# Optimization experiments

Measured on AMD Instinct MI355X. Metric: run time of the kernel, lower is better.

The kernel has to match this reference:

```python
import jax, jax.numpy as jnp
import numpy as np


def setup_inputs() -> dict:
    key = jax.random.key(0)
    ks = jax.random.split(key, 9)
    N, C, H, W, K = 8, 512, 64, 64, 32
    C4 = C // 4
    s = lambda k, shape, scale=0.02: jax.random.normal(k, shape, dtype=jnp.float32) * scale
    return {
        "x": jax.random.normal(ks[0], (N, C, H, W), dtype=jnp.float32),
        "y": jax.random.normal(ks[1], (N, K, C), dtype=jnp.float32),
        "wq": s(ks[2], (C4, C)),
        "bq": s(ks[3], (C4,)),
        "wk": s(ks[4], (C4, C)),
        "bk": s(ks[5], (C4,)),
        "wv": s(ks[6], (C, C)),
        "bv": s(ks[7], (C,)),
        "scale": s(ks[8], (1,), 1.0),
    }


def reference(x, y, wq, bq, wk, bk, wv, bv, scale):
    N, C, H, W = x.shape
    # 1x1 conv query: (N,C,H,W) -> (N,C4,H,W) -> (N, HW, C4)
    q = jnp.einsum('nchw,oc->nhwo', x, wq) + bq  # (N,H,W,C4)
    q = q.reshape(N, H * W, -1)                   # (N, HW, C4)
    # key/value linears on centers y: (N,K,C)
    k = y @ wk.T + bk                             # (N, K, C4)
    v = y @ wv.T + bv                             # (N, K, C)
    energy = jnp.einsum('npc,nkc->npk', q, k)     # (N, HW, K)
    attn = jax.nn.softmax(energy, axis=-1)
    out = jnp.einsum('nkc,npk->ncp', v, attn)     # (N, C, HW)
    out = out.reshape(N, C, H, W)
    return scale[0] * out + x
```

## Files before the change

### kernel.cpp

```cpp
#include <hip/hip_runtime.h>


#define N_  8
#define C_  512
#define HW_ 4096
#define K_  32

typedef __attribute__((ext_vector_type(8))) short bf16x8;
typedef __attribute__((ext_vector_type(4))) float f32x4;
typedef __attribute__((ext_vector_type(4))) int i32x4;

__device__ __forceinline__ unsigned short f2b(float f) {
    union { float f; unsigned u; } v; v.f = f;
    unsigned r = v.u + 0x7FFFu + ((v.u >> 16) & 1u);
    return (unsigned short)(r >> 16);
}

__device__ __forceinline__ int wqk_idx(int kk, int c) {
    return ((((c >> 5) * 2 + (kk >> 4)) * 64 + ((c >> 3) & 3) * 16 + (kk & 15)) << 3) + (c & 7);
}

__global__ __launch_bounds__(256) void prep_kernel(
    const float* __restrict__ y, const float* __restrict__ wq, const float* __restrict__ bq,
    const float* __restrict__ wk, const float* __restrict__ bk,
    const float* __restrict__ wv, const float* __restrict__ bv,
    unsigned short* __restrict__ wqkf, float* __restrict__ bqk, float* __restrict__ vp)
{
    const int bid = blockIdx.x;
    const int t = threadIdx.x;

    if (bid < 128) {
        const int n  = bid >> 4;
        const int ct = (bid >> 1) & 7;
        const int jh = bid & 1;
        const int cl = t & 63;
        const int c  = ct * 64 + cl;
        const int kko = __builtin_amdgcn_readfirstlane(t >> 6);

        const float* yb  = y  + ((size_t)n * K_ + kko * 8) * C_ + jh * 256;
        const float* wvb = wv + (size_t)c * C_ + jh * 256;
        float acc[8] = {0,0,0,0,0,0,0,0};
        for (int jq = 0; jq < 64; ++jq) {
            float4 w4 = *(const float4*)(wvb + jq * 4);
            #pragma unroll
            for (int u = 0; u < 8; ++u) {
                float4 y4 = *(const float4*)(yb + (size_t)u * C_ + jq * 4);
                acc[u] += y4.x * w4.x + y4.y * w4.y + y4.z * w4.z + y4.w * w4.w;
            }
        }
        const float bvc = (jh == 0) ? bv[c] : 0.0f;
        float* vpo = vp + (size_t)jh * N_ * K_ * C_;
        #pragma unroll
        for (int u = 0; u < 8; ++u)
            vpo[((size_t)n * K_ + kko * 8 + u) * C_ + c] = acc[u] + bvc;
    } else {
        __shared__ __align__(16) float kp[2][128];
        __shared__ __align__(16) float kr[128];
        const int b = bid - 128;
        const int n = b >> 5, kk = b & 31;
        const int o = t & 127, half = t >> 7;

        const float* yb  = y  + ((size_t)n * K_ + kk) * C_ + half * 256;
        const float* wkb = wk + (size_t)o * C_ + half * 256;
        float a = 0.f;
        for (int jq = 0; jq < 64; ++jq) {
            float4 w4 = *(const float4*)(wkb + jq * 4);
            float4 y4 = *(const float4*)(yb + jq * 4);
            a += y4.x * w4.x + y4.y * w4.y + y4.z * w4.z + y4.w * w4.w;
        }
        kp[half][o] = a;
        __syncthreads();
        if (t < 128) kr[t] = kp[0][t] + kp[1][t] + bk[t];
        __syncthreads();
        if (t < 64) {
            float s = kr[t] * bq[t] + kr[t + 64] * bq[t + 64];
            #pragma unroll
            for (int d = 32; d > 0; d >>= 1) s += __shfl_down(s, d);
            if (t == 0) bqk[n * K_ + kk] = s;
        }
        const int c1 = t, c2 = t + 256;
        float s1 = 0.f, s2 = 0.f;
        for (int oq = 0; oq < 32; ++oq) {
            float4 k4 = *(const float4*)(&kr[oq * 4]);
            const float* wq0 = wq + (size_t)(oq * 4) * C_;
            s1 += k4.x * wq0[c1] + k4.y * wq0[C_ + c1] + k4.z * wq0[2*C_ + c1] + k4.w * wq0[3*C_ + c1];
            s2 += k4.x * wq0[c2] + k4.y * wq0[C_ + c2] + k4.z * wq0[2*C_ + c2] + k4.w * wq0[3*C_ + c2];
        }
        unsigned short* wqf_n = wqkf + (size_t)n * (K_ * C_);
        wqf_n[wqk_idx(kk, c1)] = f2b(s1);
        wqf_n[wqk_idx(kk, c2)] = f2b(s2);
    }
}

__global__ __launch_bounds__(256) void pack_v_kernel(
    const float* __restrict__ vp, unsigned short* __restrict__ vtf)
{
    const int gid = blockIdx.x * 256 + threadIdx.x;
    const int n = gid >> 11, rem = gid & 2047;
    const int l = rem & 63;
    const int mt = rem >> 6;
    const int c = mt * 16 + (l & 15), g = l >> 4;
    const float* p0 = vp + ((size_t)n * K_ + g * 8) * C_ + c;
    const float* p1 = p0 + (size_t)N_ * K_ * C_;
    unsigned short o[8];
    #pragma unroll
    for (int j = 0; j < 8; ++j) o[j] = f2b(p0[(size_t)j * C_] + p1[(size_t)j * C_]);
    i32x4 pk = { (int)(o[0] | ((unsigned)o[1] << 16)), (int)(o[2] | ((unsigned)o[3] << 16)),
                 (int)(o[4] | ((unsigned)o[5] << 16)), (int)(o[6] | ((unsigned)o[7] << 16)) };
    *(i32x4*)(vtf + (size_t)n * (K_ * C_) + (size_t)rem * 8) = pk;
}

__global__ __launch_bounds__(512) void main_kernel(
    const float* __restrict__ x, const unsigned short* __restrict__ wqkf,
    const unsigned short* __restrict__ vtf, const float* __restrict__ bqk,
    const float* __restrict__ scale, float* __restrict__ out)
{
    __shared__ float e_lds[64][33];
    __shared__ __align__(16) unsigned short attnf[2048];

    const int bid = blockIdx.x;
    const int n  = bid >> 6;
    const int p0 = (bid & 63) * 64;
    const int t  = threadIdx.x;
    const int w  = t >> 6, l = t & 63;
    const int l15 = l & 15, lg = l >> 4;

    {
        const int pt = w & 3, kt = w >> 2;
        const unsigned short* wqf = wqkf + (size_t)n * (K_ * C_);
        const float* xc = x + (size_t)n * C_ * HW_ + p0 + pt * 16 + l15;

        float xr[8];
        #pragma unroll
        for (int u = 0; u < 8; ++u) xr[u] = xc[(size_t)(8 * lg + u) * HW_];
        bf16x8 bcur = *(const bf16x8*)(wqf + ((size_t)kt * 64 + l) * 8);

        f32x4 acc = {0.f, 0.f, 0.f, 0.f};
        for (int cs = 0; cs < 16; ++cs) {
            float xn[8];
            bf16x8 bnext;
            if (cs < 15) {
                #pragma unroll
                for (int u = 0; u < 8; ++u)
                    xn[u] = xc[(size_t)((cs + 1) * 32 + 8 * lg + u) * HW_];
                bnext = *(const bf16x8*)(wqf + ((size_t)((cs + 1) * 2 + kt) * 64 + l) * 8);
            }
            bf16x8 af;
            #pragma unroll
            for (int u = 0; u < 8; ++u) af[u] = (short)f2b(xr[u]);
            acc = __builtin_amdgcn_mfma_f32_16x16x32_bf16(af, bcur, acc, 0, 0, 0);
            #pragma unroll
            for (int u = 0; u < 8; ++u) xr[u] = xn[u];
            bcur = bnext;
        }
        const float bq_ = bqk[n * K_ + kt * 16 + l15];
        #pragma unroll
        for (int r = 0; r < 4; ++r)
            e_lds[pt * 16 + lg * 4 + r][kt * 16 + l15] = acc[r] + bq_;
    }
    __syncthreads();

    if (t < 64) {
        const int px = t;
        float e[32];
        #pragma unroll
        for (int k = 0; k < 32; ++k) e[k] = e_lds[px][k];
        float mx = e[0];
        #pragma unroll
        for (int k = 1; k < 32; ++k) mx = fmaxf(mx, e[k]);
        float s = 0.f;
        #pragma unroll
        for (int k = 0; k < 32; ++k) { e[k] = __expf(e[k] - mx); s += e[k]; }
        const float inv = 1.f / s;
        const int pt = px >> 4, c15 = px & 15;
        #pragma unroll
        for (int g = 0; g < 4; ++g) {
            i32x4 pk = { (int)(f2b(e[8*g+0]*inv) | ((unsigned)f2b(e[8*g+1]*inv) << 16)),
                         (int)(f2b(e[8*g+2]*inv) | ((unsigned)f2b(e[8*g+3]*inv) << 16)),
                         (int)(f2b(e[8*g+4]*inv) | ((unsigned)f2b(e[8*g+5]*inv) << 16)),
                         (int)(f2b(e[8*g+6]*inv) | ((unsigned)f2b(e[8*g+7]*inv) << 16)) };
            *(i32x4*)&attnf[(pt * 64 + g * 16 + c15) * 8] = pk;
        }
    }
    __syncthreads();

    {
        const int pt = w & 3, mh = w >> 2;
        const bf16x8 af = *(const bf16x8*)&attnf[(pt * 64 + l) * 8];
        const unsigned short* vtfn = vtf + (size_t)n * (K_ * C_);
        const float fs = scale[0];
        const int px = p0 + pt * 16 + l15;
        const float* xg = x + (size_t)n * C_ * HW_;
        float* og = out + (size_t)n * C_ * HW_;

        const int mt0 = mh * 16;
        bf16x8 vcur = *(const bf16x8*)(vtfn + ((size_t)mt0 * 64 + l) * 8);
        const int c0 = mt0 * 16 + lg * 4;
        float x0 = xg[(size_t)c0 * HW_ + px],       x1 = xg[(size_t)(c0+1) * HW_ + px];
        float x2 = xg[(size_t)(c0+2) * HW_ + px],   x3 = xg[(size_t)(c0+3) * HW_ + px];

        for (int mi = 0; mi < 16; ++mi) {
            const int mt = mh * 16 + mi;
            bf16x8 vnext;
            float y0, y1, y2, y3;
            if (mi < 15) {
                vnext = *(const bf16x8*)(vtfn + ((size_t)(mt + 1) * 64 + l) * 8);
                const int cn = (mt + 1) * 16 + lg * 4;
                y0 = xg[(size_t)cn * HW_ + px];       y1 = xg[(size_t)(cn+1) * HW_ + px];
                y2 = xg[(size_t)(cn+2) * HW_ + px];   y3 = xg[(size_t)(cn+3) * HW_ + px];
            }
            f32x4 d = __builtin_amdgcn_mfma_f32_16x16x32_bf16(vcur, af, (f32x4){0.f,0.f,0.f,0.f}, 0, 0, 0);
            const int cc = mt * 16 + lg * 4;
            og[(size_t)cc * HW_ + px]       = fs * d[0] + x0;
            og[(size_t)(cc+1) * HW_ + px]   = fs * d[1] + x1;
            og[(size_t)(cc+2) * HW_ + px]   = fs * d[2] + x2;
            og[(size_t)(cc+3) * HW_ + px]   = fs * d[3] + x3;
            vcur = vnext; x0 = y0; x1 = y1; x2 = y2; x3 = y3;
        }
    }
}

extern "C" void kernel_launch(void* const* d_in, const int* in_sizes, int n_in,
                              void* d_out, int out_size, void* d_ws, size_t ws_size,
                              hipStream_t stream) {
    const float* x     = (const float*)d_in[0];
    const float* y     = (const float*)d_in[1];
    const float* wq    = (const float*)d_in[2];
    const float* bq    = (const float*)d_in[3];
    const float* wk    = (const float*)d_in[4];
    const float* bk    = (const float*)d_in[5];
    const float* wv    = (const float*)d_in[6];
    const float* bv    = (const float*)d_in[7];
    const float* scale = (const float*)d_in[8];

    unsigned short* wqkf = (unsigned short*)d_ws;
    unsigned short* vtf  = wqkf + (size_t)N_ * K_ * C_;
    float* bqk = (float*)((char*)d_ws + 524288);
    float* vp  = (float*)((char*)d_ws + 525312);

    prep_kernel<<<384, 256, 0, stream>>>(y, wq, bq, wk, bk, wv, bv, wqkf, bqk, vp);
    pack_v_kernel<<<64, 256, 0, stream>>>(vp, vtf);
    main_kernel<<<N_ * 64, 512, 0, stream>>>(x, wqkf, vtf, bqk, scale, (float*)d_out);
}
```

Before: 64.19 us.

## Fuse V packing into prep, shrink main tiles to 32 pixels, softmax in all waves

The V projection no longer splits the channel reduction in half. It now writes packed bf16 V directly in the MFMA layout, which removes the pack_v kernel launch and the fp32 intermediate buffer. The main kernel processes 32 pixels per 256-thread block, giving 1024 blocks with an XCD-aware block index swizzle. Every wave now computes its own softmax rows straight into MFMA operand registers, which drops the attnf LDS staging and a barrier. The price is duplicated softmax work and fewer prep blocks on the V path, so each prep thread runs a longer serial loop.

Result: slower. 115.1 us (+79.3%).

```diff
diff --git a/kernel.cpp b/kernel.cpp
--- a/kernel.cpp
+++ b/kernel.cpp
@@ -24,23 +24,23 @@
     const float* __restrict__ y, const float* __restrict__ wq, const float* __restrict__ bq,
     const float* __restrict__ wk, const float* __restrict__ bk,
     const float* __restrict__ wv, const float* __restrict__ bv,
-    unsigned short* __restrict__ wqkf, float* __restrict__ bqk, float* __restrict__ vp)
+    unsigned short* __restrict__ wqkf, float* __restrict__ bqk, unsigned short* __restrict__ vtf)
 {
     const int bid = blockIdx.x;
     const int t = threadIdx.x;
 
-    if (bid < 128) {
-        const int n  = bid >> 4;
-        const int ct = (bid >> 1) & 7;
-        const int jh = bid & 1;
+    if (bid < 64) {
+        const int n  = bid >> 3;
+        const int ct = bid & 7;
         const int cl = t & 63;
         const int c  = ct * 64 + cl;
-        const int kko = __builtin_amdgcn_readfirstlane(t >> 6);
-
-        const float* yb  = y  + ((size_t)n * K_ + kko * 8) * C_ + jh * 256;
-        const float* wvb = wv + (size_t)c * C_ + jh * 256;
+        const int kko = t >> 6;
+
+        const float* yb  = y  + ((size_t)n * K_ + kko * 8) * C_;
+        const float* wvb = wv + (size_t)c * C_;
         float acc[8] = {0,0,0,0,0,0,0,0};
-        for (int jq = 0; jq < 64; ++jq) {
+        #pragma unroll 2
+        for (int jq = 0; jq < 128; ++jq) {
             float4 w4 = *(const float4*)(wvb + jq * 4);
             #pragma unroll
             for (int u = 0; u < 8; ++u) {
@@ -48,21 +48,25 @@
                 acc[u] += y4.x * w4.x + y4.y * w4.y + y4.z * w4.z + y4.w * w4.w;
             }
         }
-        const float bvc = (jh == 0) ? bv[c] : 0.0f;
-        float* vpo = vp + (size_t)jh * N_ * K_ * C_;
-        #pragma unroll
-        for (int u = 0; u < 8; ++u)
-            vpo[((size_t)n * K_ + kko * 8 + u) * C_ + c] = acc[u] + bvc;
+        const float bvc = bv[c];
+        unsigned short o[8];
+        #pragma unroll
+        for (int u = 0; u < 8; ++u) o[u] = f2b(acc[u] + bvc);
+        i32x4 pk = { (int)(o[0] | ((unsigned)o[1] << 16)), (int)(o[2] | ((unsigned)o[3] << 16)),
+                     (int)(o[4] | ((unsigned)o[5] << 16)), (int)(o[6] | ((unsigned)o[7] << 16)) };
+        *(i32x4*)(vtf + (size_t)n * (K_ * C_) +
+                  (size_t)(((c >> 4) * 64 + kko * 16 + (c & 15)) * 8)) = pk;
     } else {
         __shared__ __align__(16) float kp[2][128];
         __shared__ __align__(16) float kr[128];
-        const int b = bid - 128;
+        const int b = bid - 64;
         const int n = b >> 5, kk = b & 31;
         const int o = t & 127, half = t >> 7;
 
         const float* yb  = y  + ((size_t)n * K_ + kk) * C_ + half * 256;
         const float* wkb = wk + (size_t)o * C_ + half * 256;
         float a = 0.f;
+        #pragma unroll 4
         for (int jq = 0; jq < 64; ++jq) {
             float4 w4 = *(const float4*)(wkb + jq * 4);
             float4 y4 = *(const float4*)(yb + jq * 4);
@@ -92,66 +96,59 @@
     }
 }
 
-__global__ __launch_bounds__(256) void pack_v_kernel(
-    const float* __restrict__ vp, unsigned short* __restrict__ vtf)
-{
-    const int gid = blockIdx.x * 256 + threadIdx.x;
-    const int n = gid >> 11, rem = gid & 2047;
-    const int l = rem & 63;
-    const int mt = rem >> 6;
-    const int c = mt * 16 + (l & 15), g = l >> 4;
-    const float* p0 = vp + ((size_t)n * K_ + g * 8) * C_ + c;
-    const float* p1 = p0 + (size_t)N_ * K_ * C_;
-    unsigned short o[8];
-    #pragma unroll
-    for (int j = 0; j < 8; ++j) o[j] = f2b(p0[(size_t)j * C_] + p1[(size_t)j * C_]);
-    i32x4 pk = { (int)(o[0] | ((unsigned)o[1] << 16)), (int)(o[2] | ((unsigned)o[3] << 16)),
-                 (int)(o[4] | ((unsigned)o[5] << 16)), (int)(o[6] | ((unsigned)o[7] << 16)) };
-    *(i32x4*)(vtf + (size_t)n * (K_ * C_) + (size_t)rem * 8) = pk;
-}
-
-__global__ __launch_bounds__(512) void main_kernel(
+__global__ __launch_bounds__(256) void main_kernel(
     const float* __restrict__ x, const unsigned short* __restrict__ wqkf,
     const unsigned short* __restrict__ vtf, const float* __restrict__ bqk,
     const float* __restrict__ scale, float* __restrict__ out)
 {
-    __shared__ float e_lds[64][33];
-    __shared__ __align__(16) unsigned short attnf[2048];
-
-    const int bid = blockIdx.x;
-    const int n  = bid >> 6;
-    const int p0 = (bid & 63) * 64;
+    __shared__ float e_lds[32][33];
+
+    const int bid = (blockIdx.x & 7) * 128 + (blockIdx.x >> 3);
+    const int n  = bid >> 7;
+    const int p0 = (bid & 127) * 32;
     const int t  = threadIdx.x;
     const int w  = t >> 6, l = t & 63;
     const int l15 = l & 15, lg = l >> 4;
+    const float* xg = x + (size_t)n * C_ * HW_;
+    float* og = out + (size_t)n * C_ * HW_;
 
     {
-        const int pt = w & 3, kt = w >> 2;
+        const int pt = w & 1, kt = w >> 1;
         const unsigned short* wqf = wqkf + (size_t)n * (K_ * C_);
-        const float* xc = x + (size_t)n * C_ * HW_ + p0 + pt * 16 + l15;
-
-        float xr[8];
-        #pragma unroll
-        for (int u = 0; u < 8; ++u) xr[u] = xc[(size_t)(8 * lg + u) * HW_];
-        bf16x8 bcur = *(const bf16x8*)(wqf + ((size_t)kt * 64 + l) * 8);
+        const float* xc = xg + p0 + pt * 16 + l15;
+
+        float xr0[8], xr1[8];
+        #pragma unroll
+        for (int u = 0; u < 8; ++u) xr0[u] = xc[(size_t)(8 * lg + u) * HW_];
+        #pragma unroll
+        for (int u = 0; u < 8; ++u) xr1[u] = xc[(size_t)(32 + 8 * lg + u) * HW_];
+        bf16x8 b0 = *(const bf16x8*)(wqf + ((size_t)(0 + kt) * 64 + l) * 8);
+        bf16x8 b1 = *(const bf16x8*)(wqf + ((size_t)(2 + kt) * 64 + l) * 8);
 
         f32x4 acc = {0.f, 0.f, 0.f, 0.f};
-        for (int cs = 0; cs < 16; ++cs) {
-            float xn[8];
-            bf16x8 bnext;
-            if (cs < 15) {
+        for (int cs = 0; cs < 16; cs += 2) {
+            float xn0[8], xn1[8];
+            bf16x8 bn0, bn1;
+            if (cs < 14) {
                 #pragma unroll
                 for (int u = 0; u < 8; ++u)
-                    xn[u] = xc[(size_t)((cs + 1) * 32 + 8 * lg + u) * HW_];
-                bnext = *(const bf16x8*)(wqf + ((size_t)((cs + 1) * 2 + kt) * 64 + l) * 8);
+                    xn0[u] = xc[(size_t)((cs + 2) * 32 + 8 * lg + u) * HW_];
+                bn0 = *(const bf16x8*)(wqf + ((size_t)((cs + 2) * 2 + kt) * 64 + l) * 8);
+                #pragma unroll
+                for (int u = 0; u < 8; ++u)
+                    xn1[u] = xc[(size_t)((cs + 3) * 32 + 8 * lg + u) * HW_];
+                bn1 = *(const bf16x8*)(wqf + ((size_t)((cs + 3) * 2 + kt) * 64 + l) * 8);
             }
-            bf16x8 af;
-            #pragma unroll
-            for (int u = 0; u < 8; ++u) af[u] = (short)f2b(xr[u]);
-            acc = __builtin_amdgcn_mfma_f32_16x16x32_bf16(af, bcur, acc, 0, 0, 0);
-            #pragma unroll
-            for (int u = 0; u < 8; ++u) xr[u] = xn[u];
-            bcur = bnext;
+            bf16x8 af0, af1;
+            #pragma unroll
+            for (int u = 0; u < 8; ++u) af0[u] = (short)f2b(xr0[u]);
+            acc = __builtin_amdgcn_mfma_f32_16x16x32_bf16(af0, b0, acc, 0, 0, 0);
+            #pragma unroll
+            for (int u = 0; u < 8; ++u) af1[u] = (short)f2b(xr1[u]);
+            acc = __builtin_amdgcn_mfma_f32_16x16x32_bf16(af1, b1, acc, 0, 0, 0);
+            #pragma unroll
+            for (int u = 0; u < 8; ++u) { xr0[u] = xn0[u]; xr1[u] = xn1[u]; }
+            b0 = bn0; b1 = bn1;
         }
         const float bq_ = bqk[n * K_ + kt * 16 + l15];
         #pragma unroll
@@ -160,11 +157,13 @@
     }
     __syncthreads();
 
-    if (t < 64) {
-        const int px = t;
+    bf16x8 paf;
+    {
+        const int pxt = w & 1;
+        const float* er = e_lds[pxt * 16 + l15];
         float e[32];
         #pragma unroll
-        for (int k = 0; k < 32; ++k) e[k] = e_lds[px][k];
+        for (int k = 0; k < 32; ++k) e[k] = er[k];
         float mx = e[0];
         #pragma unroll
         for (int k = 1; k < 32; ++k) mx = fmaxf(mx, e[k]);
@@ -172,26 +171,15 @@
         #pragma unroll
         for (int k = 0; k < 32; ++k) { e[k] = __expf(e[k] - mx); s += e[k]; }
         const float inv = 1.f / s;
-        const int pt = px >> 4, c15 = px & 15;
-        #pragma unroll
-        for (int g = 0; g < 4; ++g) {
-            i32x4 pk = { (int)(f2b(e[8*g+0]*inv) | ((unsigned)f2b(e[8*g+1]*inv) << 16)),
-                         (int)(f2b(e[8*g+2]*inv) | ((unsigned)f2b(e[8*g+3]*inv) << 16)),
-                         (int)(f2b(e[8*g+4]*inv) | ((unsigned)f2b(e[8*g+5]*inv) << 16)),
-                         (int)(f2b(e[8*g+6]*inv) | ((unsigned)f2b(e[8*g+7]*inv) << 16)) };
-            *(i32x4*)&attnf[(pt * 64 + g * 16 + c15) * 8] = pk;
-        }
-    }
-    __syncthreads();
+        #pragma unroll
+        for (int j = 0; j < 8; ++j) paf[j] = (short)f2b(e[8 * lg + j] * inv);
+    }
 
     {
-        const int pt = w & 3, mh = w >> 2;
-        const bf16x8 af = *(const bf16x8*)&attnf[(pt * 64 + l) * 8];
+        const int pxt = w & 1, mh = w >> 1;
         const unsigned short* vtfn = vtf + (size_t)n * (K_ * C_);
         const float fs = scale[0];
-        const int px = p0 + pt * 16 + l15;
-        const float* xg = x + (size_t)n * C_ * HW_;
-        float* og = out + (size_t)n * C_ * HW_;
+        const int px = p0 + pxt * 16 + l15;
 
         const int mt0 = mh * 16;
         bf16x8 vcur = *(const bf16x8*)(vtfn + ((size_t)mt0 * 64 + l) * 8);
@@ -209,7 +197,7 @@
                 y0 = xg[(size_t)cn * HW_ + px];       y1 = xg[(size_t)(cn+1) * HW_ + px];
                 y2 = xg[(size_t)(cn+2) * HW_ + px];   y3 = xg[(size_t)(cn+3) * HW_ + px];
             }
-            f32x4 d = __builtin_amdgcn_mfma_f32_16x16x32_bf16(vcur, af, (f32x4){0.f,0.f,0.f,0.f}, 0, 0, 0);
+            f32x4 d = __builtin_amdgcn_mfma_f32_16x16x32_bf16(vcur, paf, (f32x4){0.f,0.f,0.f,0.f}, 0, 0, 0);
             const int cc = mt * 16 + lg * 4;
             og[(size_t)cc * HW_ + px]       = fs * d[0] + x0;
             og[(size_t)(cc+1) * HW_ + px]   = fs * d[1] + x1;
@@ -236,9 +224,7 @@
     unsigned short* wqkf = (unsigned short*)d_ws;
     unsigned short* vtf  = wqkf + (size_t)N_ * K_ * C_;
     float* bqk = (float*)((char*)d_ws + 524288);
-    float* vp  = (float*)((char*)d_ws + 525312);
-
-    prep_kernel<<<384, 256, 0, stream>>>(y, wq, bq, wk, bk, wv, bv, wqkf, bqk, vp);
-    pack_v_kernel<<<64, 256, 0, stream>>>(vp, vtf);
-    main_kernel<<<N_ * 64, 512, 0, stream>>>(x, wqkf, vtf, bqk, scale, (float*)d_out);
-}
+
+    prep_kernel<<<320, 256, 0, stream>>>(y, wq, bq, wk, bk, wv, bv, wqkf, bqk, vtf);
+    main_kernel<<<1024, 256, 0, stream>>>(x, wqkf, vtf, bqk, scale, (float*)d_out);
+}
```
